# Performance work log

Hardware: AMD Instinct MI355X
Metric: run time of the kernel (lower is better)

Reference implementation:

```python
import jax, jax.numpy as jnp
import numpy as np

B, N, H = 1024, 4096, 32


def setup_inputs() -> dict:
    key = jax.random.key(0)
    ks = jax.random.split(key, 9)
    node_embedding = jax.random.normal(ks[0], (B, N, H), dtype=jnp.float32)
    mask = jax.random.randint(ks[1], (B, N), 0, 2).astype(jnp.float32)
    times = jax.random.uniform(ks[2], (B,), dtype=jnp.float32)
    idxc = jax.random.randint(ks[3], (B, 1), 0, N)
    # parameters
    vf = jax.random.uniform(ks[4], (1, H), dtype=jnp.float32)
    lim1 = 1.0 / np.sqrt(2 * H + 1)
    W1 = jax.random.uniform(ks[5], (H, 2 * H + 1), minval=-lim1, maxval=lim1, dtype=jnp.float32)
    b1 = jax.random.uniform(ks[6], (H,), minval=-lim1, maxval=lim1, dtype=jnp.float32)
    limh = 1.0 / np.sqrt(H)
    Wq = jax.random.uniform(ks[7], (H, H), minval=-limh, maxval=limh, dtype=jnp.float32)
    Wk = jax.random.uniform(ks[8], (H, H), minval=-limh, maxval=limh, dtype=jnp.float32)
    return {"node_embedding": node_embedding, "mask": mask, "times": times,
            "vf": vf, "W1": W1, "b1": b1, "Wq": Wq, "Wk": Wk, "idxc": idxc}


def reference(node_embedding, mask, times, vf, W1, b1, Wq, Wk, idxc):
    h = node_embedding.shape[-1]
    node_avg = jnp.mean(node_embedding, axis=1)                       # [B, H]
    # gather per-batch context node (idxc path; vf used only when idxc is None)
    f = jnp.take_along_axis(node_embedding, idxc[:, :, None], axis=1)[:, 0, :]  # [B, H]
    cat = jnp.concatenate([node_avg, f, times[:, None]], axis=1)      # [B, 2H+1]
    emb = cat @ W1.T + b1                                             # [B, H]
    q = emb @ Wq.T                                                    # [B, H]
    k = node_embedding @ Wk.T                                         # [B, N, H]
    scores = jnp.einsum('bh,bnh->bn', q, k) / jnp.sqrt(jnp.asarray(h, emb.dtype))
    scores = scores - mask * 999999999.0
    return jax.nn.softmax(scores, axis=-1)
```

## Files before the change

kernel.cpp:

```cpp
#include <hip/hip_runtime.h>
#include <math.h>

#define BB 1024
#define NN 4096
#define HH 32
#define PP 4
#define RK1 (NN / PP)
#define QQ 4
#define RQ (NN / QQ)

#define WS_PART 0
#define WS_QK   (BB * PP * HH)
#define WS_MS   (WS_QK + BB * HH)

__global__ __launch_bounds__(256) void k1_colsum(
    const float* __restrict__ ne, float* __restrict__ ws)
{
    const int blk = blockIdx.x;
    const int b   = blk >> 2;
    const int p   = blk & (PP - 1);
    const int tid = threadIdx.x;
    const int q8  = tid & 7;
    const int r   = tid >> 3;

    __shared__ float s_part[256 * 4];

    const float* base = ne + (size_t)b * (NN * HH)
                           + (size_t)(p * RK1 + r) * HH + q8 * 4;
    float a0 = 0.f, a1 = 0.f, a2 = 0.f, a3 = 0.f;
    #pragma unroll 8
    for (int i = 0; i < RK1 / 32; ++i) {
        const float4 v = *reinterpret_cast<const float4*>(base + i * (32 * HH));
        a0 += v.x; a1 += v.y; a2 += v.z; a3 += v.w;
    }
    *reinterpret_cast<float4*>(&s_part[tid * 4]) = make_float4(a0, a1, a2, a3);
    __syncthreads();

    if (tid < HH) {
        const int q = tid >> 2, j = tid & 3;
        float s = 0.f;
        #pragma unroll
        for (int rr = 0; rr < 32; ++rr) s += s_part[(rr * 8 + q) * 4 + j];
        ws[WS_PART + (b * PP + p) * HH + tid] = s;
    }
}

__global__ __launch_bounds__(64) void k2_mlp(
    const float* __restrict__ ne, const float* __restrict__ times,
    const float* __restrict__ W1, const float* __restrict__ b1,
    const float* __restrict__ Wq, const float* __restrict__ Wk,
    const int* __restrict__ idxc, float* __restrict__ ws)
{
    const int b   = blockIdx.x;
    const int tid = threadIdx.x;
    __shared__ float sh_avg[HH], sh_f[HH], sh_emb[HH], sh_q[HH];

    if (tid < HH) {
        float s = 0.f;
        #pragma unroll
        for (int p = 0; p < PP; ++p) s += ws[WS_PART + (b * PP + p) * HH + tid];
        sh_avg[tid] = s * (1.0f / (float)NN);
        sh_f[tid]   = ne[(size_t)b * (NN * HH) + (size_t)idxc[b] * HH + tid];
    }
    __syncthreads();
    if (tid < HH) {
        const float t = times[b];
        const float* w = W1 + tid * (2 * HH + 1);
        float e = b1[tid];
        #pragma unroll
        for (int j = 0; j < HH; ++j) e += sh_avg[j] * w[j];
        #pragma unroll
        for (int j = 0; j < HH; ++j) e += sh_f[j] * w[HH + j];
        e += t * w[2 * HH];
        sh_emb[tid] = e;
    }
    __syncthreads();
    if (tid < HH) {
        const float* w = Wq + tid * HH;
        float qv = 0.f;
        #pragma unroll
        for (int j = 0; j < HH; ++j) qv += sh_emb[j] * w[j];
        sh_q[tid] = qv;
    }
    __syncthreads();
    if (tid < HH) {
        float s = 0.f;
        #pragma unroll
        for (int h = 0; h < HH; ++h) s += sh_q[h] * Wk[h * HH + tid];
        ws[WS_QK + b * HH + tid] = s * 0.17677669529663687f;
    }
}

__global__ __launch_bounds__(256) void k3a_scores(
    const float* __restrict__ ne, const float* __restrict__ mask,
    const float* __restrict__ ws, float* __restrict__ out,
    float* __restrict__ ws_ms)
{
    const int blk = blockIdx.x;
    const int b   = blk >> 2;
    const int q   = blk & (QQ - 1);
    const int tid = threadIdx.x;
    const int q8  = tid & 7;
    const int r   = tid >> 3;

    __shared__ float s_scores[RQ];
    __shared__ float sh_qk[HH];
    __shared__ float red_buf[4];
    __shared__ float red_sum[4];

    if (tid < HH) sh_qk[tid] = ws[WS_QK + b * HH + tid];

    const float4 mv = *reinterpret_cast<const float4*>(
        mask + (size_t)b * NN + q * RQ + tid * 4);
    __syncthreads();

    const float kq0 = sh_qk[q8 * 4 + 0];
    const float kq1 = sh_qk[q8 * 4 + 1];
    const float kq2 = sh_qk[q8 * 4 + 2];
    const float kq3 = sh_qk[q8 * 4 + 3];

    const float* base = ne + (size_t)b * (NN * HH)
                           + (size_t)(q * RQ + r) * HH + q8 * 4;

    #pragma unroll 8
    for (int i = 0; i < RQ / 32; ++i) {
        const float4 v = *reinterpret_cast<const float4*>(base + i * (32 * HH));
        float p = v.x * kq0 + v.y * kq1 + v.z * kq2 + v.w * kq3;
        p += __shfl_xor(p, 1);
        p += __shfl_xor(p, 2);
        p += __shfl_xor(p, 4);
        if (q8 == 0) s_scores[r + i * 32] = p;
    }
    __syncthreads();

    const float4 s4 = *reinterpret_cast<const float4*>(&s_scores[tid * 4]);
    float sc0 = s4.x - mv.x * 999999999.0f;
    float sc1 = s4.y - mv.y * 999999999.0f;
    float sc2 = s4.z - mv.z * 999999999.0f;
    float sc3 = s4.w - mv.w * 999999999.0f;

    float lmax = fmaxf(fmaxf(sc0, sc1), fmaxf(sc2, sc3));
    #pragma unroll
    for (int m = 1; m < 64; m <<= 1) lmax = fmaxf(lmax, __shfl_xor(lmax, m));
    if ((tid & 63) == 0) red_buf[tid >> 6] = lmax;
    __syncthreads();
    const float bmax = fmaxf(fmaxf(red_buf[0], red_buf[1]),
                             fmaxf(red_buf[2], red_buf[3]));

    const float e0 = expf(sc0 - bmax);
    const float e1 = expf(sc1 - bmax);
    const float e2 = expf(sc2 - bmax);
    const float e3 = expf(sc3 - bmax);
    float lsum = (e0 + e1) + (e2 + e3);
    #pragma unroll
    for (int m = 1; m < 64; m <<= 1) lsum += __shfl_xor(lsum, m);
    if ((tid & 63) == 0) red_sum[tid >> 6] = lsum;

    *reinterpret_cast<float4*>(out + (size_t)b * NN + q * RQ + tid * 4) =
        make_float4(e0, e1, e2, e3);

    __syncthreads();
    if (tid == 0) {
        const float bsum = (red_sum[0] + red_sum[1]) + (red_sum[2] + red_sum[3]);
        ws_ms[(b * QQ + q) * 2 + 0] = bmax;
        ws_ms[(b * QQ + q) * 2 + 1] = bsum;
    }
}

__global__ __launch_bounds__(256) void k3b_rescale(
    const float* __restrict__ ws_ms, float* __restrict__ out)
{
    const int blk = blockIdx.x;
    const int b   = blk >> 2;
    const int q   = blk & (QQ - 1);
    const int tid = threadIdx.x;

    const float m0 = ws_ms[(b * QQ + 0) * 2 + 0], s0 = ws_ms[(b * QQ + 0) * 2 + 1];
    const float m1 = ws_ms[(b * QQ + 1) * 2 + 0], s1 = ws_ms[(b * QQ + 1) * 2 + 1];
    const float m2 = ws_ms[(b * QQ + 2) * 2 + 0], s2 = ws_ms[(b * QQ + 2) * 2 + 1];
    const float m3 = ws_ms[(b * QQ + 3) * 2 + 0], s3 = ws_ms[(b * QQ + 3) * 2 + 1];

    const float M = fmaxf(fmaxf(m0, m1), fmaxf(m2, m3));
    const float S = s0 * expf(m0 - M) + s1 * expf(m1 - M)
                  + s2 * expf(m2 - M) + s3 * expf(m3 - M);
    const float mq = (q == 0) ? m0 : (q == 1) ? m1 : (q == 2) ? m2 : m3;
    const float scale = expf(mq - M) / S;

    float* p = out + (size_t)b * NN + q * RQ + tid * 4;
    const float4 v = *reinterpret_cast<const float4*>(p);
    *reinterpret_cast<float4*>(p) =
        make_float4(v.x * scale, v.y * scale, v.z * scale, v.w * scale);
}

extern "C" void kernel_launch(void* const* d_in, const int* in_sizes, int n_in,
                              void* d_out, int out_size, void* d_ws, size_t ws_size,
                              hipStream_t stream) {
    (void)in_sizes; (void)n_in; (void)ws_size; (void)out_size;
    const float* ne    = (const float*)d_in[0];
    const float* mask  = (const float*)d_in[1];
    const float* times = (const float*)d_in[2];
    const float* W1    = (const float*)d_in[4];
    const float* b1    = (const float*)d_in[5];
    const float* Wq    = (const float*)d_in[6];
    const float* Wk    = (const float*)d_in[7];
    const int*   idxc  = (const int*)d_in[8];
    float* out = (float*)d_out;
    float* ws  = (float*)d_ws;

    k1_colsum<<<dim3(BB * PP), dim3(256), 0, stream>>>(ne, ws);
    k2_mlp<<<dim3(BB), dim3(64), 0, stream>>>(ne, times, W1, b1, Wq, Wk, idxc, ws);
    k3a_scores<<<dim3(BB * QQ), dim3(256), 0, stream>>>(ne, mask, ws, out, ws + WS_MS);
    k3b_rescale<<<dim3(BB * QQ), dim3(256), 0, stream>>>(ws + WS_MS, out);
}
```

Measured before the change: 213.2 us.

## Pipeline column-sum and score stages across batch chunks in one fused kernel

Merges the column-sum, MLP and score kernels into one kernel that is launched once per batch chunk. Each launch runs the column sum for chunk d next to the scores for chunk d-1, and every score block recomputes the small MLP itself. The goal is to overlap the two streaming passes over node_embedding, hide the small serial MLP kernel, and possibly reuse chunk data left in L2. The cost is nine launches instead of three, redundant MLP work in every score block, and a skewed per-launch workload that may leave the GPU underused.

New measurement: 272.2 us. +27.6%, slower.

```diff
diff --git a/kernel.cpp b/kernel.cpp
--- a/kernel.cpp
+++ b/kernel.cpp
@@ -8,52 +8,79 @@
 #define RK1 (NN / PP)
 #define QQ 4
 #define RQ (NN / QQ)
+#define CHUNK 128
+#define NCH (BB / CHUNK)
+#define K1B (CHUNK * PP)
+#define K3B (CHUNK * QQ)
 
 #define WS_PART 0
-#define WS_QK   (BB * PP * HH)
-#define WS_MS   (WS_QK + BB * HH)
-
-__global__ __launch_bounds__(256) void k1_colsum(
-    const float* __restrict__ ne, float* __restrict__ ws)
+#define WS_MS   (BB * PP * HH)
+
+__global__ __launch_bounds__(256) void pipe(
+    const float* __restrict__ ne,
+    const float* __restrict__ mask,
+    const float* __restrict__ times,
+    const float* __restrict__ W1,
+    const float* __restrict__ b1,
+    const float* __restrict__ Wq,
+    const float* __restrict__ Wk,
+    const int*   __restrict__ idxc,
+    float* __restrict__ ws,
+    float* __restrict__ out,
+    float* __restrict__ ws_ms,
+    int k1c, int k3c)
 {
-    const int blk = blockIdx.x;
-    const int b   = blk >> 2;
-    const int p   = blk & (PP - 1);
+    __shared__ float smem[RK1 + 160];
     const int tid = threadIdx.x;
+
+    if ((int)blockIdx.x < K1B) {
+        if (k1c < 0) return;
+        const int blk = blockIdx.x;
+        const int b   = k1c * CHUNK + (blk >> 2);
+        const int p   = blk & (PP - 1);
+        const int q8  = tid & 7;
+        const int r   = tid >> 3;
+
+        float* s_part = smem;
+
+        const float* base = ne + (size_t)b * (NN * HH)
+                               + (size_t)(p * RK1 + r) * HH + q8 * 4;
+        float a0 = 0.f, a1 = 0.f, a2 = 0.f, a3 = 0.f;
+        #pragma unroll 8
+        for (int i = 0; i < RK1 / 32; ++i) {
+            const float4 v = *reinterpret_cast<const float4*>(base + i * (32 * HH));
+            a0 += v.x; a1 += v.y; a2 += v.z; a3 += v.w;
+        }
+        *reinterpret_cast<float4*>(&s_part[tid * 4]) = make_float4(a0, a1, a2, a3);
+        __syncthreads();
+
+        if (tid < HH) {
+            const int qq = tid >> 2, j = tid & 3;
+            float s = 0.f;
+            #pragma unroll
+            for (int rr = 0; rr < 32; ++rr) s += s_part[(rr * 8 + qq) * 4 + j];
+            ws[WS_PART + (b * PP + p) * HH + tid] = s;
+        }
+        return;
+    }
+
+    if (k3c < 0) return;
+    const int j2  = (int)blockIdx.x - K1B;
+    const int b   = k3c * CHUNK + (j2 >> 2);
+    const int qi  = j2 & (QQ - 1);
     const int q8  = tid & 7;
     const int r   = tid >> 3;
 
-    __shared__ float s_part[256 * 4];
-
-    const float* base = ne + (size_t)b * (NN * HH)
-                           + (size_t)(p * RK1 + r) * HH + q8 * 4;
-    float a0 = 0.f, a1 = 0.f, a2 = 0.f, a3 = 0.f;
-    #pragma unroll 8
-    for (int i = 0; i < RK1 / 32; ++i) {
-        const float4 v = *reinterpret_cast<const float4*>(base + i * (32 * HH));
-        a0 += v.x; a1 += v.y; a2 += v.z; a3 += v.w;
-    }
-    *reinterpret_cast<float4*>(&s_part[tid * 4]) = make_float4(a0, a1, a2, a3);
-    __syncthreads();
-
-    if (tid < HH) {
-        const int q = tid >> 2, j = tid & 3;
-        float s = 0.f;
-        #pragma unroll
-        for (int rr = 0; rr < 32; ++rr) s += s_part[(rr * 8 + q) * 4 + j];
-        ws[WS_PART + (b * PP + p) * HH + tid] = s;
-    }
-}
-
-__global__ __launch_bounds__(64) void k2_mlp(
-    const float* __restrict__ ne, const float* __restrict__ times,
-    const float* __restrict__ W1, const float* __restrict__ b1,
-    const float* __restrict__ Wq, const float* __restrict__ Wk,
-    const int* __restrict__ idxc, float* __restrict__ ws)
-{
-    const int b   = blockIdx.x;
-    const int tid = threadIdx.x;
-    __shared__ float sh_avg[HH], sh_f[HH], sh_emb[HH], sh_q[HH];
+    float* s_scores = smem;
+    float* sh_avg   = smem + RQ;
+    float* sh_f     = smem + RQ + 32;
+    float* sh_emb   = smem + RQ + 64;
+    float* sh_qk    = smem + RQ + 96;
+    float* red_buf  = smem + RQ + 128;
+    float* red_sum  = smem + RQ + 136;
+
+    const float4 mv = *reinterpret_cast<const float4*>(
+        mask + (size_t)b * NN + qi * RQ + tid * 4);
 
     if (tid < HH) {
         float s = 0.f;
@@ -80,38 +107,15 @@
         float qv = 0.f;
         #pragma unroll
         for (int j = 0; j < HH; ++j) qv += sh_emb[j] * w[j];
-        sh_q[tid] = qv;
+        sh_f[tid] = qv;
     }
     __syncthreads();
     if (tid < HH) {
         float s = 0.f;
         #pragma unroll
-        for (int h = 0; h < HH; ++h) s += sh_q[h] * Wk[h * HH + tid];
-        ws[WS_QK + b * HH + tid] = s * 0.17677669529663687f;
-    }
-}
-
-__global__ __launch_bounds__(256) void k3a_scores(
-    const float* __restrict__ ne, const float* __restrict__ mask,
-    const float* __restrict__ ws, float* __restrict__ out,
-    float* __restrict__ ws_ms)
-{
-    const int blk = blockIdx.x;
-    const int b   = blk >> 2;
-    const int q   = blk & (QQ - 1);
-    const int tid = threadIdx.x;
-    const int q8  = tid & 7;
-    const int r   = tid >> 3;
-
-    __shared__ float s_scores[RQ];
-    __shared__ float sh_qk[HH];
-    __shared__ float red_buf[4];
-    __shared__ float red_sum[4];
-
-    if (tid < HH) sh_qk[tid] = ws[WS_QK + b * HH + tid];
-
-    const float4 mv = *reinterpret_cast<const float4*>(
-        mask + (size_t)b * NN + q * RQ + tid * 4);
+        for (int h = 0; h < HH; ++h) s += sh_f[h] * Wk[h * HH + tid];
+        sh_qk[tid] = s * 0.17677669529663687f;
+    }
     __syncthreads();
 
     const float kq0 = sh_qk[q8 * 4 + 0];
@@ -120,7 +124,7 @@
     const float kq3 = sh_qk[q8 * 4 + 3];
 
     const float* base = ne + (size_t)b * (NN * HH)
-                           + (size_t)(q * RQ + r) * HH + q8 * 4;
+                           + (size_t)(qi * RQ + r) * HH + q8 * 4;
 
     #pragma unroll 8
     for (int i = 0; i < RQ / 32; ++i) {
@@ -134,10 +138,10 @@
     __syncthreads();
 
     const float4 s4 = *reinterpret_cast<const float4*>(&s_scores[tid * 4]);
-    float sc0 = s4.x - mv.x * 999999999.0f;
-    float sc1 = s4.y - mv.y * 999999999.0f;
-    float sc2 = s4.z - mv.z * 999999999.0f;
-    float sc3 = s4.w - mv.w * 999999999.0f;
+    const float sc0 = s4.x - mv.x * 999999999.0f;
+    const float sc1 = s4.y - mv.y * 999999999.0f;
+    const float sc2 = s4.z - mv.z * 999999999.0f;
+    const float sc3 = s4.w - mv.w * 999999999.0f;
 
     float lmax = fmaxf(fmaxf(sc0, sc1), fmaxf(sc2, sc3));
     #pragma unroll
@@ -156,14 +160,14 @@
     for (int m = 1; m < 64; m <<= 1) lsum += __shfl_xor(lsum, m);
     if ((tid & 63) == 0) red_sum[tid >> 6] = lsum;
 
-    *reinterpret_cast<float4*>(out + (size_t)b * NN + q * RQ + tid * 4) =
+    *reinterpret_cast<float4*>(out + (size_t)b * NN + qi * RQ + tid * 4) =
         make_float4(e0, e1, e2, e3);
 
     __syncthreads();
     if (tid == 0) {
         const float bsum = (red_sum[0] + red_sum[1]) + (red_sum[2] + red_sum[3]);
-        ws_ms[(b * QQ + q) * 2 + 0] = bmax;
-        ws_ms[(b * QQ + q) * 2 + 1] = bsum;
+        ws_ms[(b * QQ + qi) * 2 + 0] = bmax;
+        ws_ms[(b * QQ + qi) * 2 + 1] = bsum;
     }
 }
 
@@ -172,7 +176,7 @@
 {
     const int blk = blockIdx.x;
     const int b   = blk >> 2;
-    const int q   = blk & (QQ - 1);
+    const int qi  = blk & (QQ - 1);
     const int tid = threadIdx.x;
 
     const float m0 = ws_ms[(b * QQ + 0) * 2 + 0], s0 = ws_ms[(b * QQ + 0) * 2 + 1];
@@ -183,10 +187,10 @@
     const float M = fmaxf(fmaxf(m0, m1), fmaxf(m2, m3));
     const float S = s0 * expf(m0 - M) + s1 * expf(m1 - M)
                   + s2 * expf(m2 - M) + s3 * expf(m3 - M);
-    const float mq = (q == 0) ? m0 : (q == 1) ? m1 : (q == 2) ? m2 : m3;
+    const float mq = (qi == 0) ? m0 : (qi == 1) ? m1 : (qi == 2) ? m2 : m3;
     const float scale = expf(mq - M) / S;
 
-    float* p = out + (size_t)b * NN + q * RQ + tid * 4;
+    float* p = out + (size_t)b * NN + qi * RQ + tid * 4;
     const float4 v = *reinterpret_cast<const float4*>(p);
     *reinterpret_cast<float4*>(p) =
         make_float4(v.x * scale, v.y * scale, v.z * scale, v.w * scale);
@@ -207,8 +211,11 @@
     float* out = (float*)d_out;
     float* ws  = (float*)d_ws;
 
-    k1_colsum<<<dim3(BB * PP), dim3(256), 0, stream>>>(ne, ws);
-    k2_mlp<<<dim3(BB), dim3(64), 0, stream>>>(ne, times, W1, b1, Wq, Wk, idxc, ws);
-    k3a_scores<<<dim3(BB * QQ), dim3(256), 0, stream>>>(ne, mask, ws, out, ws + WS_MS);
+    for (int d = 0; d <= NCH; ++d) {
+        const int k1c = (d < NCH) ? d : -1;
+        const int k3c = d - 1;
+        pipe<<<dim3(K1B + K3B), dim3(256), 0, stream>>>(
+            ne, mask, times, W1, b1, Wq, Wk, idxc, ws, out, ws + WS_MS, k1c, k3c);
+    }
     k3b_rescale<<<dim3(BB * QQ), dim3(256), 0, stream>>>(ws + WS_MS, out);
 }
```
